# Performance work log

Measured on AMD Instinct MI355X. Metric: run time of the kernel, lower is better.

## Reference

```python
import jax, jax.numpy as jnp
import numpy as np

B, S, H, E, K = 4, 2048, 1024, 8, 2


def setup_inputs() -> dict:
    key = jax.random.key(0)
    k0, k1, k2 = jax.random.split(key, 3)
    x = jax.random.normal(k0, (B, S, H), dtype=jnp.float32)
    # gate: Linear(H -> E); torch stores W as [out,in], we keep [E,H]
    gate_w = jax.random.normal(k1, (E, H), dtype=jnp.float32) * 0.02
    gate_b = jnp.zeros((E,), dtype=jnp.float32)
    # experts: E x Linear(H -> H); stored as [E, H_in, H_out]
    expert_w = jax.random.normal(k2, (E, H, H), dtype=jnp.float32) * 0.02
    expert_b = jnp.zeros((E, H), dtype=jnp.float32)
    return {"x": x, "gate_w": gate_w, "gate_b": gate_b,
            "expert_w": expert_w, "expert_b": expert_b}


def reference(x, gate_w, gate_b, expert_w, expert_b):
    bsz, seq_len, h = x.shape
    xt = x.reshape(-1, h)                      # [T, H]
    T = xt.shape[0]

    # router (moe_router): softmax -> top-k -> renormalize
    logits = xt @ gate_w.T + gate_b            # [T, E]
    routing_probs = jax.nn.softmax(logits, axis=-1)
    top_k_probs, top_k_index = jax.lax.top_k(routing_probs, K)
    top_k_probs = top_k_probs / jnp.sum(top_k_probs, axis=1, keepdims=True)
    top_k_probs = top_k_probs.astype(x.dtype)

    # combine weights: scatter normalized top-k probs into [T, E]
    rows = jnp.arange(T)[:, None]
    combine = jnp.zeros((T, E), dtype=x.dtype).at[rows, top_k_index].add(top_k_probs)

    # per-expert FFN over all tokens, then weighted combine
    # (equivalent math to the gather / index_add loop: zero weights contribute zero)
    y = jnp.einsum('th,eho->teo', xt, expert_w) + expert_b[None, :, :]  # [T, E, H]
    out = jnp.einsum('te,teh->th', combine, y)                          # [T, H]

    final_output = out.reshape(bsz, seq_len, h)
    return final_output, top_k_index, routing_probs
```

## Files before the change

### kernel.cpp

```cpp
#include <hip/hip_runtime.h>
#include <hip/hip_bf16.h>
#include <stdint.h>

typedef unsigned short ushort_t;
typedef __bf16 bf16x8 __attribute__((ext_vector_type(8)));
typedef float f32x4 __attribute__((ext_vector_type(4)));

#define T_TOK 8192
#define H_DIM 1024
#define E_EXP 8
#define BM 128
#define BN 128
#define BK 64
#define NKT (H_DIM / BK)
#define NITER (NKT / 2)
#define NWG_G 1280

#define CNT_STRIDE 64
#define RTOK 32
#define RBLOCKS (T_TOK / RTOK)
#define TP_BLOCKS ((H_DIM / 32) * (H_DIM / 32) * E_EXP)

static __device__ __forceinline__ ushort_t f2bf(float f) {
  union { float f; uint32_t u; } c; c.f = f;
  uint32_t u = c.u;
  uint32_t r = u + 0x7FFFu + ((u >> 16) & 1u);
  return (ushort_t)(r >> 16);
}

__global__ __launch_bounds__(256) void router_transpose(
    const float* __restrict__ x, const float* __restrict__ gw,
    const float* __restrict__ gb, const float* __restrict__ ew,
    float* __restrict__ out_idx, float* __restrict__ out_probs,
    int* __restrict__ counts, int* __restrict__ tok, float* __restrict__ wts,
    ushort_t* __restrict__ xg, ushort_t* __restrict__ wT)
{
  __shared__ ushort_t xrow[RTOK][H_DIM];
  __shared__ int   sm_eid[RTOK * 2];
  __shared__ float sm_wt[RTOK * 2];
  __shared__ int   sm_dst[RTOK * 2];
  __shared__ int   lcnt[E_EXP], lbase[E_EXP], lpos[E_EXP];
  __shared__ float tile[32][33];

  const int tid = threadIdx.x;

  if (blockIdx.x >= RBLOCKS) {
    const int tb = blockIdx.x - RBLOCKS;
    const int e = tb >> 10;
    const int n0 = (tb & 31) * 32, k0 = ((tb >> 5) & 31) * 32;
    const float* we = ew + (size_t)e * H_DIM * H_DIM;
    ushort_t* wTe = wT + (size_t)e * H_DIM * H_DIM;
    const int tx = tid & 31, ty = tid >> 5;
#pragma unroll
    for (int i = 0; i < 4; i++)
      tile[ty + 8 * i][tx] = we[(size_t)(k0 + ty + 8 * i) * H_DIM + n0 + tx];
    __syncthreads();
#pragma unroll
    for (int i = 0; i < 4; i++)
      wTe[(size_t)(n0 + ty + 8 * i) * H_DIM + k0 + tx] = f2bf(tile[tx][ty + 8 * i]);
    return;
  }

  const int wave = tid >> 6, l = tid & 63;
  if (tid < E_EXP) { lcnt[tid] = 0; lpos[tid] = 0; }
  __syncthreads();

  const int t0 = blockIdx.x * RTOK;
  for (int it = 0; it < RTOK / 4; it++) {
    const int lt = wave * (RTOK / 4) + it;
    const int t = t0 + lt;
    const float* xt = x + (size_t)t * H_DIM;
    float acc[E_EXP];
#pragma unroll
    for (int e = 0; e < E_EXP; e++) acc[e] = 0.f;
#pragma unroll
    for (int i = 0; i < 4; i++) {
      const int h = (i * 64 + l) * 4;
      const float4 xv = *reinterpret_cast<const float4*>(xt + h);
      ushort4 b;
      b.x = f2bf(xv.x); b.y = f2bf(xv.y); b.z = f2bf(xv.z); b.w = f2bf(xv.w);
      *reinterpret_cast<ushort4*>(&xrow[lt][h]) = b;
#pragma unroll
      for (int e = 0; e < E_EXP; e++) {
        const float4 g = *reinterpret_cast<const float4*>(gw + e * H_DIM + h);
        acc[e] += xv.x * g.x + xv.y * g.y + xv.z * g.z + xv.w * g.w;
      }
    }
#pragma unroll
    for (int e = 0; e < E_EXP; e++) {
      float v = acc[e];
#pragma unroll
      for (int off = 32; off; off >>= 1) v += __shfl_xor(v, off);
      acc[e] = v;
    }
    if (l == 0) {
      float lg[E_EXP], pb[E_EXP];
      float m = -1e30f;
#pragma unroll
      for (int e = 0; e < E_EXP; e++) { lg[e] = acc[e] + gb[e]; m = fmaxf(m, lg[e]); }
      float s = 0.f;
#pragma unroll
      for (int e = 0; e < E_EXP; e++) { pb[e] = expf(lg[e] - m); s += pb[e]; }
      const float inv = 1.f / s;
#pragma unroll
      for (int e = 0; e < E_EXP; e++) {
        pb[e] *= inv;
        out_probs[(size_t)t * E_EXP + e] = pb[e];
      }
      int i0 = 0; float p0 = pb[0];
#pragma unroll
      for (int e = 1; e < E_EXP; e++) if (pb[e] > p0) { p0 = pb[e]; i0 = e; }
      int i1 = -1; float p1 = -1.f;
#pragma unroll
      for (int e = 0; e < E_EXP; e++) if (e != i0 && pb[e] > p1) { p1 = pb[e]; i1 = e; }
      out_idx[(size_t)t * 2 + 0] = (float)i0;
      out_idx[(size_t)t * 2 + 1] = (float)i1;
      const float rn = 1.f / (p0 + p1);
      sm_eid[lt * 2 + 0] = i0; sm_wt[lt * 2 + 0] = p0 * rn;
      sm_eid[lt * 2 + 1] = i1; sm_wt[lt * 2 + 1] = p1 * rn;
    }
  }
  __syncthreads();

  if (tid < RTOK * 2) atomicAdd(&lcnt[sm_eid[tid]], 1);
  __syncthreads();
  if (tid < E_EXP) lbase[tid] = atomicAdd(&counts[tid * CNT_STRIDE], lcnt[tid]);
  __syncthreads();
  if (tid < RTOK * 2) {
    const int e = sm_eid[tid];
    const int p = lbase[e] + atomicAdd(&lpos[e], 1);
    const int dst = e * T_TOK + p;
    tok[dst] = (t0 + (tid >> 1)) * 2 + (tid & 1);
    wts[dst] = sm_wt[tid];
    sm_dst[tid] = dst;
  }
  __syncthreads();

  for (int ent0 = 0; ent0 < RTOK * 2; ent0 += 4) {
    const int ent = ent0 + wave;
    const int dst = sm_dst[ent];
    const ushort_t* src = &xrow[ent >> 1][0];
    ushort_t* d = xg + (size_t)dst * H_DIM;
    const int o = l * 16;
    *reinterpret_cast<int4*>(d + o) = *reinterpret_cast<const int4*>(src + o);
    *reinterpret_cast<int4*>(d + o + 8) =
        *reinterpret_cast<const int4*>(src + o + 8);
  }
}

#define GLDS16(gp, lp)                                                         \
  __builtin_amdgcn_global_load_lds(                                            \
      (const __attribute__((address_space(1))) void*)(gp),                     \
      (__attribute__((address_space(3))) void*)(lp), 16, 0, 0)

#define WAITV6() asm volatile("s_waitcnt vmcnt(6)" ::: "memory")
#define WAITV0() asm volatile("s_waitcnt vmcnt(0)" ::: "memory")
#define LGKM0()                                                                \
  do {                                                                         \
    asm volatile("s_waitcnt lgkmcnt(0)" ::: "memory");                         \
    __builtin_amdgcn_sched_barrier(0);                                         \
  } while (0)
#define BAR()                                                                  \
  do {                                                                         \
    __builtin_amdgcn_sched_barrier(0);                                         \
    __builtin_amdgcn_s_barrier();                                              \
    __builtin_amdgcn_sched_barrier(0);                                         \
  } while (0)

__global__ __launch_bounds__(256, 2) void moe_gemm(
    const ushort_t* __restrict__ xg, const ushort_t* __restrict__ wT,
    const float* __restrict__ bias, int* __restrict__ counts,
    const int* __restrict__ tok, const float* __restrict__ wts,
    ushort_t* __restrict__ y)
{
  __shared__ __align__(16) ushort_t AsR[2 * 2 * BM * 32];
  __shared__ __align__(16) ushort_t BsR[2 * 2 * BM * 32];
  __shared__ int stok[BM];
  __shared__ float swt[BM];
  __shared__ int s_spill;
#define AS_(buf, kh, idx) AsR[((buf) * 2 + (kh)) * 4096 + (idx)]
#define BS_(buf, kh, idx) BsR[((buf) * 2 + (kh)) * 4096 + (idx)]

  const int tid = threadIdx.x;
  const int bid = blockIdx.x;

  int ne[E_EXP], fl[E_EXP];
#pragma unroll
  for (int i = 0; i < E_EXP; i++) {
    ne[i] = counts[i * CNT_STRIDE];
    fl[i] = ne[i] >> 7;
  }

  const int l = tid & 63;
  const int wid = tid >> 6;
  const int fr = l & 15;
  const int g = l >> 4;

  if (bid < 1024) {
    int e = bid & 7;
    int q = bid >> 3;
    const int home = fl[e] * 8;
    if (q >= (home < 128 ? home : 128)) {
      int sc[E_EXP], spill_total = 0;
#pragma unroll
      for (int i = 0; i < E_EXP; i++) {
        sc[i] = fl[i] * 8 > 128 ? fl[i] * 8 - 128 : 0;
        spill_total += sc[i];
      }
      if (spill_total == 0) return;
      if (tid == 0) s_spill = atomicAdd(&counts[520], 1);
      __syncthreads();
      int k = s_spill;
      if (k >= spill_total) return;
      int done = 0;
#pragma unroll
      for (int i = 0; i < E_EXP; i++) {
        if (!done) { if (k < sc[i]) { e = i; done = 1; } else k -= sc[i]; }
      }
      q = 128 + k;
    }
    const int mt = q >> 3;
    const int nt = q & 7;

    if (tid < BM) {
      stok[tid] = tok[e * T_TOK + mt * BM + tid];
      swt[tid] = wts[e * T_TOK + mt * BM + tid];
    }
    __syncthreads();

    const int r0 = tid >> 2;
    const int cp = (tid & 3) ^ ((tid >> 3) & 3);
    const ushort_t* wTe = wT + (size_t)e * H_DIM * H_DIM;
    const ushort_t* aBase = xg + (size_t)(e * T_TOK + mt * BM) * H_DIM;
    const ushort_t* aP0 = aBase + (size_t)r0 * H_DIM + cp * 8;
    const ushort_t* aP1 = aBase + (size_t)(r0 + 64) * H_DIM + cp * 8;
    const ushort_t* bP0 = wTe + (size_t)(nt * BN + r0) * H_DIM + cp * 8;
    const ushort_t* bP1 = wTe + (size_t)(nt * BN + r0 + 64) * H_DIM + cp * 8;
    const int d0 = tid * 8;
    const int d1 = (tid + 256) * 8;

#define STAGE_A(t, kh, buf)                                                    \
  do {                                                                         \
    GLDS16(aP0 + (t) * BK + (kh) * 32, &AS_((buf), (kh), d0));                 \
    GLDS16(aP1 + (t) * BK + (kh) * 32, &AS_((buf), (kh), d1));                 \
  } while (0)
#define STAGE_B(t, kh, buf)                                                    \
  do {                                                                         \
    GLDS16(bP0 + (t) * BK + (kh) * 32, &BS_((buf), (kh), d0));                 \
    GLDS16(bP1 + (t) * BK + (kh) * 32, &BS_((buf), (kh), d1));                 \
  } while (0)

    const int wm = wid >> 1, wn = wid & 1;
    const int sl = g ^ ((l >> 1) & 3);
    const int arow0 = wm * 64 + fr;
    const int brow0 = wn * 64 + fr;

    bf16x8 af[4], bv[2];
    f32x4 acc[4][4] = {};

#define READ_A(buf, kk)                                                        \
  do {                                                                         \
    _Pragma("unroll") for (int mi = 0; mi < 4; mi++)                           \
        af[mi] = *reinterpret_cast<const bf16x8*>(                             \
            &AS_((buf), (kk), (arow0 + mi * 16) * 32 + sl * 8));               \
  } while (0)
#define READ_B(buf, kk, nh)                                                    \
  do {                                                                         \
    _Pragma("unroll") for (int j = 0; j < 2; j++)                              \
        bv[j] = *reinterpret_cast<const bf16x8*>(                              \
            &BS_((buf), (kk), (brow0 + ((nh) * 2 + j) * 16) * 32 + sl * 8));   \
  } while (0)
#define MFMA8(nh)                                                              \
  do {                                                                         \
    __builtin_amdgcn_s_setprio(1);                                             \
    _Pragma("unroll") for (int mi = 0; mi < 4; mi++)                           \
        _Pragma("unroll") for (int j = 0; j < 2; j++)                          \
            acc[mi][(nh) * 2 + j] = __builtin_amdgcn_mfma_f32_16x16x32_bf16(   \
                af[mi], bv[j], acc[mi][(nh) * 2 + j], 0, 0, 0);                \
    __builtin_amdgcn_s_setprio(0);                                             \
  } while (0)

#define ITER_BODY(TT, MORE)                                                    \
  do {                                                                         \
                                                                       \
    READ_A(0, 0); READ_B(0, 0, 0);                                             \
    STAGE_B((TT) + 1, 1, 1);                                                   \
    BAR(); LGKM0(); MFMA8(0); BAR();                                           \
                                                                       \
    READ_B(0, 0, 1);                                                           \
    if (MORE) STAGE_A((TT) + 2, 0, 0);                                         \
    BAR(); LGKM0(); MFMA8(1); BAR();                                           \
                                                                       \
    READ_A(0, 1); READ_B(0, 1, 0);                                             \
    if (MORE) STAGE_B((TT) + 2, 0, 0);                                         \
    BAR(); LGKM0(); MFMA8(0); BAR();                                           \
                                               \
    READ_B(0, 1, 1);                                                           \
    if (MORE) { STAGE_A((TT) + 2, 1, 0); WAITV6(); } else { WAITV0(); }        \
    BAR(); LGKM0(); MFMA8(1); BAR();                                           \
                                                                       \
    READ_A(1, 0); READ_B(1, 0, 0);                                             \
    if (MORE) STAGE_B((TT) + 2, 1, 0);                                         \
    BAR(); LGKM0(); MFMA8(0); BAR();                                           \
                                                                       \
    READ_B(1, 0, 1);                                                           \
    if (MORE) STAGE_A((TT) + 3, 0, 1);                                         \
    BAR(); LGKM0(); MFMA8(1); BAR();                                           \
                                                                       \
    READ_A(1, 1); READ_B(1, 1, 0);                                             \
    if (MORE) STAGE_B((TT) + 3, 0, 1);                                         \
    BAR(); LGKM0(); MFMA8(0); BAR();                                           \
                                               \
    READ_B(1, 1, 1);                                                           \
    if (MORE) { STAGE_A((TT) + 3, 1, 1); WAITV6(); }                           \
    BAR(); LGKM0(); MFMA8(1); BAR();                                           \
  } while (0)

    STAGE_A(0, 0, 0); STAGE_B(0, 0, 0); STAGE_A(0, 1, 0); STAGE_B(0, 1, 0);
    STAGE_A(1, 0, 1); STAGE_B(1, 0, 1); STAGE_A(1, 1, 1);
    WAITV6();
    BAR();

#pragma unroll 1
    for (int it = 0; it < NITER - 1; ++it) {
      const int t = 2 * it;
      ITER_BODY(t, 1);
    }
    {
      const int t = 2 * (NITER - 1);
      ITER_BODY(t, 0);
    }

    float bias4[4];
#pragma unroll
    for (int nj = 0; nj < 4; nj++)
      bias4[nj] = bias[e * H_DIM + nt * BN + wn * 64 + nj * 16 + fr];
#pragma unroll
    for (int mi = 0; mi < 4; mi++) {
      const int rr0 = wm * 64 + mi * 16 + g * 4;
#pragma unroll
      for (int r = 0; r < 4; r++) {
        const int row = rr0 + r;
        const float wgt = swt[row];
        ushort_t* yr = y + (size_t)stok[row] * H_DIM;
#pragma unroll
        for (int nj = 0; nj < 4; nj++) {
          const int n = nt * BN + wn * 64 + nj * 16 + fr;
          yr[n] = f2bf(wgt * (acc[mi][nj][r] + bias4[nj]));
        }
      }
    }
  } else {
    const int e = bid & 7;
    const int tq = (bid - 1024) >> 3;
    const int rem = ne[e] - (fl[e] << 7);
    const int tcnt = (rem + 63) >> 6;
    if (tq >= tcnt * 8) return;
    const int mtt = tq >> 3;
    const int ntt = tq & 7;
    const int row0 = (fl[e] << 7) + mtt * 64;
    int valid = ne[e] - row0; if (valid > 64) valid = 64;

    if (tid < 64) {
      int slot = row0 + tid;
      if (slot >= ne[e]) slot = ne[e] - 1;
      stok[tid] = tok[e * T_TOK + slot];
      swt[tid] = wts[e * T_TOK + slot];
    }
    __syncthreads();

    const ushort_t* wTe = wT + (size_t)e * H_DIM * H_DIM;
    const int trow = tid >> 3;
    const int tlc = (tid & 7) ^ (trow & 7);
    int tsl0 = row0 + trow;       if (tsl0 >= ne[e]) tsl0 = ne[e] - 1;
    int tsl1 = row0 + trow + 32;  if (tsl1 >= ne[e]) tsl1 = ne[e] - 1;
    const ushort_t* taS0 = xg + (size_t)(e * T_TOK + tsl0) * H_DIM + tlc * 8;
    const ushort_t* taS1 = xg + (size_t)(e * T_TOK + tsl1) * H_DIM + tlc * 8;
    const ushort_t* tbS0 = wTe + (size_t)(ntt * 128 + trow) * H_DIM + tlc * 8;
    const ushort_t* tbS1 = tbS0 + (size_t)32 * H_DIM;
    const ushort_t* tbS2 = tbS0 + (size_t)64 * H_DIM;
    const ushort_t* tbS3 = tbS0 + (size_t)96 * H_DIM;

#define TSTAGE(t, buf)                                                         \
  do {                                                                         \
    GLDS16(taS0 + (t) * BK, &AsR[(buf) * 4096 + tid * 8]);                     \
    GLDS16(taS1 + (t) * BK, &AsR[(buf) * 4096 + (tid + 256) * 8]);             \
    GLDS16(tbS0 + (t) * BK, &BsR[(buf) * 8192 + tid * 8]);                     \
    GLDS16(tbS1 + (t) * BK, &BsR[(buf) * 8192 + (tid + 256) * 8]);             \
    GLDS16(tbS2 + (t) * BK, &BsR[(buf) * 8192 + (tid + 512) * 8]);             \
    GLDS16(tbS3 + (t) * BK, &BsR[(buf) * 8192 + (tid + 768) * 8]);             \
  } while (0)

    const int tph0 = (g ^ (fr & 7)) * 8;
    const int tph1 = ((4 ^ g) ^ (fr & 7)) * 8;

    f32x4 tacc[2][4] = {};

    TSTAGE(0, 0);
    WAITV0();
    BAR();

#pragma unroll
    for (int t = 0; t < NKT; ++t) {
      if (t + 1 < NKT) TSTAGE(t + 1, (t + 1) & 1);
      const ushort_t* Ab = &AsR[(t & 1) * 4096];
      const ushort_t* Bb = &BsR[(t & 1) * 8192];
#pragma unroll
      for (int kk = 0; kk < 2; kk++) {
        const int ph = kk ? tph1 : tph0;
#pragma unroll
        for (int nf = 0; nf < 2; nf++) {
          const bf16x8 tbv = *reinterpret_cast<const bf16x8*>(
              &Bb[(wid * 32 + nf * 16 + fr) * 64 + ph]);
#pragma unroll
          for (int mi = 0; mi < 4; mi++) {
            const bf16x8 tav = *reinterpret_cast<const bf16x8*>(
                &Ab[(mi * 16 + fr) * 64 + ph]);
            tacc[nf][mi] = __builtin_amdgcn_mfma_f32_16x16x32_bf16(
                tav, tbv, tacc[nf][mi], 0, 0, 0);
          }
        }
      }
      WAITV0();
      BAR();
    }

#pragma unroll
    for (int nf = 0; nf < 2; nf++) {
      const int ncol = ntt * 128 + wid * 32 + nf * 16 + fr;
      const float bs = bias[e * H_DIM + ncol];
#pragma unroll
      for (int mi = 0; mi < 4; mi++) {
        const int rb = mi * 16 + g * 4;
#pragma unroll
        for (int r = 0; r < 4; r++) {
          const int row = rb + r;
          if (row < valid) {
            ushort_t* yr = y + (size_t)stok[row] * H_DIM;
            yr[ncol] = f2bf(swt[row] * (tacc[nf][mi][r] + bs));
          }
        }
      }
    }
  }
}

__global__ __launch_bounds__(256) void combine_kernel(
    const ushort_t* __restrict__ y, float* __restrict__ out)
{
  const int t = blockIdx.x;
  const ushort_t* r0 = y + (size_t)(t * 2) * H_DIM;
  const ushort_t* r1 = r0 + H_DIM;
  float* o = out + (size_t)t * H_DIM;
  const int h = threadIdx.x * 4;
  const ushort4 u0 = *reinterpret_cast<const ushort4*>(r0 + h);
  const ushort4 u1 = *reinterpret_cast<const ushort4*>(r1 + h);
  float4 v;
  union { uint32_t u; float f; } c;
  c.u = (uint32_t)u0.x << 16; v.x = c.f; c.u = (uint32_t)u1.x << 16; v.x += c.f;
  c.u = (uint32_t)u0.y << 16; v.y = c.f; c.u = (uint32_t)u1.y << 16; v.y += c.f;
  c.u = (uint32_t)u0.z << 16; v.z = c.f; c.u = (uint32_t)u1.z << 16; v.z += c.f;
  c.u = (uint32_t)u0.w << 16; v.w = c.f; c.u = (uint32_t)u1.w << 16; v.w += c.f;
  *reinterpret_cast<float4*>(o + h) = v;
}

extern "C" void kernel_launch(void* const* d_in, const int* in_sizes, int n_in,
                              void* d_out, int out_size, void* d_ws, size_t ws_size,
                              hipStream_t stream)
{
  const float* x  = (const float*)d_in[0];
  const float* gw = (const float*)d_in[1];
  const float* gb = (const float*)d_in[2];
  const float* ew = (const float*)d_in[3];
  const float* eb = (const float*)d_in[4];

  float* out = (float*)d_out;
  float* out_final = out;
  float* out_idx   = out + (size_t)T_TOK * H_DIM;
  float* out_probs = out_idx + (size_t)T_TOK * 2;

  char* ws = (char*)d_ws;
  size_t off = 0;
  int*      counts  = (int*)(ws + off); off += 4096;
  int*      tok     = (int*)(ws + off); off += (size_t)E_EXP * T_TOK * 4;
  float*    wts     = (float*)(ws + off); off += (size_t)E_EXP * T_TOK * 4;
  ushort_t* wT      = (ushort_t*)(ws + off); off += (size_t)E_EXP * H_DIM * H_DIM * 2;
  ushort_t* y       = (ushort_t*)(ws + off); off += (size_t)T_TOK * 2 * H_DIM * 2;
  ushort_t* xg      = (ushort_t*)(ws + off); off += (size_t)E_EXP * T_TOK * H_DIM * 2;

  hipMemsetAsync(counts, 0, 4096, stream);

  router_transpose<<<RBLOCKS + TP_BLOCKS, 256, 0, stream>>>(
      x, gw, gb, ew, out_idx, out_probs, counts, tok, wts, xg, wT);
  moe_gemm<<<NWG_G, 256, 0, stream>>>(xg, wT, eb, counts, tok, wts, y);
  combine_kernel<<<T_TOK, 256, 0, stream>>>(y, out_final);
}
```

Measured before the change: 107.2 us.

## Replace hand-pipelined double-buffered GEMM with single-buffer loop at higher occupancy

Removes the explicit double-buffered, hand-scheduled LDS pipeline (staged halves, vmcnt waits, many barriers) from both the main and tail GEMM paths. Each uses a single shared buffer with load, sync, compute per k-step. LDS usage halves, so launch bounds move to 3 workgroups per CU and the grid grows to 2048 main blocks plus the tail region. Latency hiding now relies on other resident waves instead of in-block prefetch, at the cost of losing overlap of global loads with MFMA inside a block.

```diff
diff --git a/kernel.cpp b/kernel.cpp
--- a/kernel.cpp
+++ b/kernel.cpp
@@ -13,8 +13,7 @@
 #define BN 128
 #define BK 64
 #define NKT (H_DIM / BK)
-#define NITER (NKT / 2)
-#define NWG_G 1280
+#define NWG_G 2304
 
 #define CNT_STRIDE 64
 #define RTOK 32
@@ -153,33 +152,17 @@
       (const __attribute__((address_space(1))) void*)(gp),                     \
       (__attribute__((address_space(3))) void*)(lp), 16, 0, 0)
 
-#define WAITV6() asm volatile("s_waitcnt vmcnt(6)" ::: "memory")
-#define WAITV0() asm volatile("s_waitcnt vmcnt(0)" ::: "memory")
-#define LGKM0()                                                                \
-  do {                                                                         \
-    asm volatile("s_waitcnt lgkmcnt(0)" ::: "memory");                         \
-    __builtin_amdgcn_sched_barrier(0);                                         \
-  } while (0)
-#define BAR()                                                                  \
-  do {                                                                         \
-    __builtin_amdgcn_sched_barrier(0);                                         \
-    __builtin_amdgcn_s_barrier();                                              \
-    __builtin_amdgcn_sched_barrier(0);                                         \
-  } while (0)
-
-__global__ __launch_bounds__(256, 2) void moe_gemm(
+__global__ __launch_bounds__(256, 3) void moe_gemm(
     const ushort_t* __restrict__ xg, const ushort_t* __restrict__ wT,
     const float* __restrict__ bias, int* __restrict__ counts,
     const int* __restrict__ tok, const float* __restrict__ wts,
     ushort_t* __restrict__ y)
 {
-  __shared__ __align__(16) ushort_t AsR[2 * 2 * BM * 32];
-  __shared__ __align__(16) ushort_t BsR[2 * 2 * BM * 32];
+  __shared__ __align__(16) ushort_t As[2 * 4096];
+  __shared__ __align__(16) ushort_t Bs[2 * 4096];
   __shared__ int stok[BM];
   __shared__ float swt[BM];
   __shared__ int s_spill;
-#define AS_(buf, kh, idx) AsR[((buf) * 2 + (kh)) * 4096 + (idx)]
-#define BS_(buf, kh, idx) BsR[((buf) * 2 + (kh)) * 4096 + (idx)]
 
   const int tid = threadIdx.x;
   const int bid = blockIdx.x;
@@ -196,15 +179,15 @@
   const int fr = l & 15;
   const int g = l >> 4;
 
-  if (bid < 1024) {
+  if (bid < 2048) {
     int e = bid & 7;
     int q = bid >> 3;
     const int home = fl[e] * 8;
-    if (q >= (home < 128 ? home : 128)) {
+    if (q >= (home < 256 ? home : 256)) {
       int sc[E_EXP], spill_total = 0;
 #pragma unroll
       for (int i = 0; i < E_EXP; i++) {
-        sc[i] = fl[i] * 8 > 128 ? fl[i] * 8 - 128 : 0;
+        sc[i] = fl[i] * 8 > 256 ? fl[i] * 8 - 256 : 0;
         spill_total += sc[i];
       }
       if (spill_total == 0) return;
@@ -217,7 +200,7 @@
       for (int i = 0; i < E_EXP; i++) {
         if (!done) { if (k < sc[i]) { e = i; done = 1; } else k -= sc[i]; }
       }
-      q = 128 + k;
+      q = 256 + k;
     }
     const int mt = q >> 3;
     const int nt = q & 7;
@@ -239,15 +222,16 @@
     const int d0 = tid * 8;
     const int d1 = (tid + 256) * 8;
 
-#define STAGE_A(t, kh, buf)                                                    \
+#define STAGE8(t)                                                              \
   do {                                                                         \
-    GLDS16(aP0 + (t) * BK + (kh) * 32, &AS_((buf), (kh), d0));                 \
-    GLDS16(aP1 + (t) * BK + (kh) * 32, &AS_((buf), (kh), d1));                 \
-  } while (0)
-#define STAGE_B(t, kh, buf)                                                    \
-  do {                                                                         \
-    GLDS16(bP0 + (t) * BK + (kh) * 32, &BS_((buf), (kh), d0));                 \
-    GLDS16(bP1 + (t) * BK + (kh) * 32, &BS_((buf), (kh), d1));                 \
+    GLDS16(aP0 + (t) * BK +  0, &As[0 * 4096 + d0]);                           \
+    GLDS16(aP1 + (t) * BK +  0, &As[0 * 4096 + d1]);                           \
+    GLDS16(aP0 + (t) * BK + 32, &As[1 * 4096 + d0]);                           \
+    GLDS16(aP1 + (t) * BK + 32, &As[1 * 4096 + d1]);                           \
+    GLDS16(bP0 + (t) * BK +  0, &Bs[0 * 4096 + d0]);                           \
+    GLDS16(bP1 + (t) * BK +  0, &Bs[0 * 4096 + d1]);                           \
+    GLDS16(bP0 + (t) * BK + 32, &Bs[1 * 4096 + d0]);                           \
+    GLDS16(bP1 + (t) * BK + 32, &Bs[1 * 4096 + d1]);                           \
   } while (0)
 
     const int wm = wid >> 1, wn = wid & 1;
@@ -255,80 +239,33 @@
     const int arow0 = wm * 64 + fr;
     const int brow0 = wn * 64 + fr;
 
-    bf16x8 af[4], bv[2];
     f32x4 acc[4][4] = {};
 
-#define READ_A(buf, kk)                                                        \
-  do {                                                                         \
-    _Pragma("unroll") for (int mi = 0; mi < 4; mi++)                           \
-        af[mi] = *reinterpret_cast<const bf16x8*>(                             \
-            &AS_((buf), (kk), (arow0 + mi * 16) * 32 + sl * 8));               \
-  } while (0)
-#define READ_B(buf, kk, nh)                                                    \
-  do {                                                                         \
-    _Pragma("unroll") for (int j = 0; j < 2; j++)                              \
-        bv[j] = *reinterpret_cast<const bf16x8*>(                              \
-            &BS_((buf), (kk), (brow0 + ((nh) * 2 + j) * 16) * 32 + sl * 8));   \
-  } while (0)
-#define MFMA8(nh)                                                              \
-  do {                                                                         \
-    __builtin_amdgcn_s_setprio(1);                                             \
-    _Pragma("unroll") for (int mi = 0; mi < 4; mi++)                           \
-        _Pragma("unroll") for (int j = 0; j < 2; j++)                          \
-            acc[mi][(nh) * 2 + j] = __builtin_amdgcn_mfma_f32_16x16x32_bf16(   \
-                af[mi], bv[j], acc[mi][(nh) * 2 + j], 0, 0, 0);                \
-    __builtin_amdgcn_s_setprio(0);                                             \
-  } while (0)
-
-#define ITER_BODY(TT, MORE)                                                    \
-  do {                                                                         \
-                                                                       \
-    READ_A(0, 0); READ_B(0, 0, 0);                                             \
-    STAGE_B((TT) + 1, 1, 1);                                                   \
-    BAR(); LGKM0(); MFMA8(0); BAR();                                           \
-                                                                       \
-    READ_B(0, 0, 1);                                                           \
-    if (MORE) STAGE_A((TT) + 2, 0, 0);                                         \
-    BAR(); LGKM0(); MFMA8(1); BAR();                                           \
-                                                                       \
-    READ_A(0, 1); READ_B(0, 1, 0);                                             \
-    if (MORE) STAGE_B((TT) + 2, 0, 0);                                         \
-    BAR(); LGKM0(); MFMA8(0); BAR();                                           \
-                                               \
-    READ_B(0, 1, 1);                                                           \
-    if (MORE) { STAGE_A((TT) + 2, 1, 0); WAITV6(); } else { WAITV0(); }        \
-    BAR(); LGKM0(); MFMA8(1); BAR();                                           \
-                                                                       \
-    READ_A(1, 0); READ_B(1, 0, 0);                                             \
-    if (MORE) STAGE_B((TT) + 2, 1, 0);                                         \
-    BAR(); LGKM0(); MFMA8(0); BAR();                                           \
-                                                                       \
-    READ_B(1, 0, 1);                                                           \
-    if (MORE) STAGE_A((TT) + 3, 0, 1);                                         \
-    BAR(); LGKM0(); MFMA8(1); BAR();                                           \
-                                                                       \
-    READ_A(1, 1); READ_B(1, 1, 0);                                             \
-    if (MORE) STAGE_B((TT) + 3, 0, 1);                                         \
-    BAR(); LGKM0(); MFMA8(0); BAR();                                           \
-                                               \
-    READ_B(1, 1, 1);                                                           \
-    if (MORE) { STAGE_A((TT) + 3, 1, 1); WAITV6(); }                           \
-    BAR(); LGKM0(); MFMA8(1); BAR();                                           \
-  } while (0)
-
-    STAGE_A(0, 0, 0); STAGE_B(0, 0, 0); STAGE_A(0, 1, 0); STAGE_B(0, 1, 0);
-    STAGE_A(1, 0, 1); STAGE_B(1, 0, 1); STAGE_A(1, 1, 1);
-    WAITV6();
-    BAR();
-
 #pragma unroll 1
-    for (int it = 0; it < NITER - 1; ++it) {
-      const int t = 2 * it;
-      ITER_BODY(t, 1);
-    }
-    {
-      const int t = 2 * (NITER - 1);
-      ITER_BODY(t, 0);
+    for (int t = 0; t < NKT; ++t) {
+      if (t) __syncthreads();
+      STAGE8(t);
+      __syncthreads();
+#pragma unroll
+      for (int kk = 0; kk < 2; kk++) {
+        bf16x8 af[4], bv[4];
+#pragma unroll
+        for (int mi = 0; mi < 4; mi++)
+          af[mi] = *reinterpret_cast<const bf16x8*>(
+              &As[kk * 4096 + (arow0 + mi * 16) * 32 + sl * 8]);
+#pragma unroll
+        for (int nj = 0; nj < 4; nj++)
+          bv[nj] = *reinterpret_cast<const bf16x8*>(
+              &Bs[kk * 4096 + (brow0 + nj * 16) * 32 + sl * 8]);
+        __builtin_amdgcn_s_setprio(1);
+#pragma unroll
+        for (int mi = 0; mi < 4; mi++)
+#pragma unroll
+          for (int nj = 0; nj < 4; nj++)
+            acc[mi][nj] = __builtin_amdgcn_mfma_f32_16x16x32_bf16(
+                af[mi], bv[nj], acc[mi][nj], 0, 0, 0);
+        __builtin_amdgcn_s_setprio(0);
+      }
     }
 
     float bias4[4];
@@ -352,7 +289,7 @@
     }
   } else {
     const int e = bid & 7;
-    const int tq = (bid - 1024) >> 3;
+    const int tq = (bid - 2048) >> 3;
     const int rem = ne[e] - (fl[e] << 7);
     const int tcnt = (rem + 63) >> 6;
     if (tq >= tcnt * 8) return;
@@ -381,14 +318,14 @@
     const ushort_t* tbS2 = tbS0 + (size_t)64 * H_DIM;
     const ushort_t* tbS3 = tbS0 + (size_t)96 * H_DIM;
 
-#define TSTAGE(t, buf)                                                         \
+#define TSTAGE1(t)                                                             \
   do {                                                                         \
-    GLDS16(taS0 + (t) * BK, &AsR[(buf) * 4096 + tid * 8]);                     \
-    GLDS16(taS1 + (t) * BK, &AsR[(buf) * 4096 + (tid + 256) * 8]);             \
-    GLDS16(tbS0 + (t) * BK, &BsR[(buf) * 8192 + tid * 8]);                     \
-    GLDS16(tbS1 + (t) * BK, &BsR[(buf) * 8192 + (tid + 256) * 8]);             \
-    GLDS16(tbS2 + (t) * BK, &BsR[(buf) * 8192 + (tid + 512) * 8]);             \
-    GLDS16(tbS3 + (t) * BK, &BsR[(buf) * 8192 + (tid + 768) * 8]);             \
+    GLDS16(taS0 + (t) * BK, &As[tid * 8]);                                     \
+    GLDS16(taS1 + (t) * BK, &As[(tid + 256) * 8]);                             \
+    GLDS16(tbS0 + (t) * BK, &Bs[tid * 8]);                                     \
+    GLDS16(tbS1 + (t) * BK, &Bs[(tid + 256) * 8]);                             \
+    GLDS16(tbS2 + (t) * BK, &Bs[(tid + 512) * 8]);                             \
+    GLDS16(tbS3 + (t) * BK, &Bs[(tid + 768) * 8]);                             \
   } while (0)
 
     const int tph0 = (g ^ (fr & 7)) * 8;
@@ -396,33 +333,27 @@
 
     f32x4 tacc[2][4] = {};
 
-    TSTAGE(0, 0);
-    WAITV0();
-    BAR();
-
-#pragma unroll
+#pragma unroll 1
     for (int t = 0; t < NKT; ++t) {
-      if (t + 1 < NKT) TSTAGE(t + 1, (t + 1) & 1);
-      const ushort_t* Ab = &AsR[(t & 1) * 4096];
-      const ushort_t* Bb = &BsR[(t & 1) * 8192];
+      if (t) __syncthreads();
+      TSTAGE1(t);
+      __syncthreads();
 #pragma unroll
       for (int kk = 0; kk < 2; kk++) {
         const int ph = kk ? tph1 : tph0;
 #pragma unroll
         for (int nf = 0; nf < 2; nf++) {
           const bf16x8 tbv = *reinterpret_cast<const bf16x8*>(
-              &Bb[(wid * 32 + nf * 16 + fr) * 64 + ph]);
+              &Bs[(wid * 32 + nf * 16 + fr) * 64 + ph]);
 #pragma unroll
           for (int mi = 0; mi < 4; mi++) {
             const bf16x8 tav = *reinterpret_cast<const bf16x8*>(
-                &Ab[(mi * 16 + fr) * 64 + ph]);
+                &As[(mi * 16 + fr) * 64 + ph]);
             tacc[nf][mi] = __builtin_amdgcn_mfma_f32_16x16x32_bf16(
                 tav, tbv, tacc[nf][mi], 0, 0, 0);
           }
         }
       }
-      WAITV0();
-      BAR();
     }
 
 #pragma unroll
```

Result: faster. 96.17 us (-10.3%).
